# Optimization experiments

Hardware: AMD Instinct MI355X
Metric: run time of the kernel (lower is better)

The kernel has to match this reference:

```python
import jax, jax.numpy as jnp
import numpy as np

DIM = 16      # model width (hardcoded in source)
HEADS = 4
DH = DIM // HEADS  # 4, per-head dim
MLP = 4
L = 4         # encoder layers
OUT = 16      # mlp_head output
EPS = 1e-5


def _ln(x, g, b):
    mu = jnp.mean(x, axis=-1, keepdims=True)
    var = jnp.mean((x - mu) ** 2, axis=-1, keepdims=True)
    return (x - mu) * jax.lax.rsqrt(var + EPS) * g + b


def setup_inputs() -> dict:
    key = jax.random.key(0)
    ks = jax.random.split(key, 16)
    B, S = 256, 512
    s = 0.1
    return {
        "x": jax.random.normal(ks[0], (B, S, DIM), jnp.float32),
        "ln1_g": jnp.ones((L, DIM), jnp.float32),
        "ln1_b": jnp.zeros((L, DIM), jnp.float32),
        "in_w": jax.random.normal(ks[1], (L, 3 * DIM, DIM), jnp.float32) * s,
        "in_b": jax.random.normal(ks[2], (L, 3 * DIM), jnp.float32) * s,
        "out_w": jax.random.normal(ks[3], (L, DIM, DIM), jnp.float32) * s,
        "out_b": jax.random.normal(ks[4], (L, DIM), jnp.float32) * s,
        "ln2_g": jnp.ones((L, DIM), jnp.float32),
        "ln2_b": jnp.zeros((L, DIM), jnp.float32),
        "w1": jax.random.normal(ks[5], (L, MLP, DIM), jnp.float32) * s,
        "b1": jax.random.normal(ks[6], (L, MLP), jnp.float32) * s,
        "w2": jax.random.normal(ks[7], (L, DIM, MLP), jnp.float32) * s,
        "b2": jax.random.normal(ks[8], (L, DIM), jnp.float32) * s,
        "head_g": jnp.ones((DIM,), jnp.float32),
        "head_b": jnp.zeros((DIM,), jnp.float32),
        "head_w": jax.random.normal(ks[9], (OUT, DIM), jnp.float32) * s,
        "head_bias": jax.random.normal(ks[10], (OUT,), jnp.float32) * s,
    }


def reference(x, ln1_g, ln1_b, in_w, in_b, out_w, out_b,
              ln2_g, ln2_b, w1, b1, w2, b2,
              head_g, head_b, head_w, head_bias):
    B, S, _ = x.shape
    scale = 1.0 / np.sqrt(DH)
    for i in range(L):
        # --- pre-LN self-attention + residual (dropout=identity at inference)
        h = _ln(x, ln1_g[i], ln1_b[i])
        qkv = h @ in_w[i].T + in_b[i]                      # [B,S,3*DIM]
        q, k, v = jnp.split(qkv, 3, axis=-1)
        q = q.reshape(B, S, HEADS, DH).transpose(0, 2, 1, 3)  # [B,H,S,Dh]
        k = k.reshape(B, S, HEADS, DH).transpose(0, 2, 1, 3)
        v = v.reshape(B, S, HEADS, DH).transpose(0, 2, 1, 3)
        scores = jnp.einsum('bhsd,bhtd->bhst', q * scale, k)  # [B,H,S,S]
        attn = jax.nn.softmax(scores, axis=-1)
        o = jnp.einsum('bhst,bhtd->bhsd', attn, v)             # [B,H,S,Dh]
        o = o.transpose(0, 2, 1, 3).reshape(B, S, DIM)
        x = x + (o @ out_w[i].T + out_b[i])
        # --- pre-LN MLP + residual (exact GELU, as torch nn.GELU default)
        h = _ln(x, ln2_g[i], ln2_b[i])
        h = jax.nn.gelu(h @ w1[i].T + b1[i], approximate=False)
        x = x + (h @ w2[i].T + b2[i])
    cls = x[:, 0, :]                                          # [B,DIM]
    return _ln(cls, head_g, head_b) @ head_w.T + head_bias    # [B,OUT]
```

## Files before the change

kernel.cpp:

```cpp
#include <hip/hip_runtime.h>
#include <math.h>

#define NDIM 16
#define NMLP 4
#define NL 4
#define NOUT 16
#define NS 512
#define NT 1024
#define LEPS 1e-5f
#define VPAD 516
#define KPAD 28

typedef __fp16 h2 __attribute__((ext_vector_type(2)));
typedef __fp16 h4 __attribute__((ext_vector_type(4)));
typedef __fp16 h8 __attribute__((ext_vector_type(8)));
typedef float f32x4 __attribute__((ext_vector_type(4)));

__device__ __forceinline__ h2 pk2(float x, float y) {
    return __builtin_amdgcn_cvt_pkrtz(x, y);
}

__device__ __forceinline__ float fexp2(float x) {
#if __has_builtin(__builtin_amdgcn_exp2f)
    return __builtin_amdgcn_exp2f(x);
#else
    return exp2f(x);
#endif
}

#define MFMA32(a,b,c) __builtin_amdgcn_mfma_f32_16x16x32_f16((a),(b),(c),0,0,0)

__global__ __launch_bounds__(NT, 4)
void vit_fused(const float* __restrict__ gx,
               const float* __restrict__ g_ln1g, const float* __restrict__ g_ln1b,
               const float* __restrict__ g_inw,  const float* __restrict__ g_inb,
               const float* __restrict__ g_outw, const float* __restrict__ g_outb,
               const float* __restrict__ g_ln2g, const float* __restrict__ g_ln2b,
               const float* __restrict__ g_w1,   const float* __restrict__ g_b1,
               const float* __restrict__ g_w2,   const float* __restrict__ g_b2,
               const float* __restrict__ g_hg,   const float* __restrict__ g_hb,
               const float* __restrict__ g_hw,   const float* __restrict__ g_hbias,
               float* __restrict__ gout)
{
    __shared__ __align__(16) __fp16 sKh[NS][KPAD];
    __shared__ __align__(16) __fp16 sVT[NDIM][VPAD];
    __shared__ __align__(16) __fp16 sQO[NS][NDIM];
    __shared__ __align__(16) float sWiw[NL*48*NDIM];
    __shared__ float sWib[NL*48];
    __shared__ __align__(16) float sWow[NL*NDIM*NDIM];
    __shared__ float sWob[NL*NDIM];
    __shared__ float sLn1g[NL*NDIM], sLn1b[NL*NDIM], sLn2g[NL*NDIM], sLn2b[NL*NDIM];
    __shared__ __align__(16) float sW1[NL*NMLP*NDIM];
    __shared__ float sB1[NL*NMLP];
    __shared__ __align__(16) float sW2[NL*NDIM*NMLP];
    __shared__ float sB2[NL*NDIM];
    __shared__ float sHg[NDIM], sHb[NDIM];
    __shared__ __align__(16) float sHw[NOUT*NDIM];
    __shared__ float sHbias[NOUT];

    const int tid = threadIdx.x;
    const int t   = tid & (NS-1);
    const int hb  = (tid >> 9) << 3;
    const int b   = blockIdx.x;

    const int w  = tid >> 6;
    const int l  = tid & 63;
    const int g  = l >> 4;
    const int ql = l & 15;
    const int r0 = 32*w;

    for (int i = tid; i < NL*48*NDIM; i += NT) sWiw[i] = g_inw[i];
    for (int i = tid; i < NL*48;       i += NT) sWib[i] = g_inb[i];
    for (int i = tid; i < NL*NDIM*NDIM; i += NT) sWow[i] = g_outw[i];
    if (tid < NL*NDIM) {
        sWob[tid]  = g_outb[tid];
        sLn1g[tid] = g_ln1g[tid];  sLn1b[tid] = g_ln1b[tid];
        sLn2g[tid] = g_ln2g[tid];  sLn2b[tid] = g_ln2b[tid];
        sB2[tid]   = g_b2[tid];
    }
    for (int i = tid; i < NL*NMLP*NDIM; i += NT) { sW1[i] = g_w1[i]; sW2[i] = g_w2[i]; }
    if (tid < NL*NMLP) sB1[tid] = g_b1[tid];
    if (tid < NDIM)  { sHg[tid] = g_hg[tid]; sHb[tid] = g_hb[tid]; }
    if (tid < NOUT)    sHbias[tid] = g_hbias[tid];
    for (int i = tid; i < NOUT*NDIM; i += NT) sHw[i] = g_hw[i];

    float xr[NDIM];
    {
        const float4* xg4 = (const float4*)(gx + ((size_t)b*NS + t)*NDIM);
        float4 a = xg4[0], b4 = xg4[1], c4 = xg4[2], d4 = xg4[3];
        xr[0]=a.x;  xr[1]=a.y;  xr[2]=a.z;  xr[3]=a.w;
        xr[4]=b4.x; xr[5]=b4.y; xr[6]=b4.z; xr[7]=b4.w;
        xr[8]=c4.x; xr[9]=c4.y; xr[10]=c4.z; xr[11]=c4.w;
        xr[12]=d4.x; xr[13]=d4.y; xr[14]=d4.z; xr[15]=d4.w;
    }

    __syncthreads();

    for (int li = 0; li < NL; ++li) {
        float mu = 0.f;
        #pragma unroll
        for (int c = 0; c < NDIM; ++c) mu += xr[c];
        mu *= (1.f/NDIM);
        float var = 0.f;
        #pragma unroll
        for (int c = 0; c < NDIM; ++c) { float d = xr[c]-mu; var += d*d; }
        var *= (1.f/NDIM);
        float rs = rsqrtf(var + LEPS);
        float hn[NDIM];
        #pragma unroll
        for (int c = 0; c < NDIM; ++c)
            hn[c] = (xr[c]-mu)*rs*sLn1g[li*NDIM+c] + sLn1b[li*NDIM+c];

        const float* iw = &sWiw[li*48*NDIM];
        const float* ib = &sWib[li*48];

        {
            const float C = 0.72134752044448170368f;
            float qf[8];
            #pragma unroll
            for (int r = 0; r < 8; ++r) {
                const float* wrow = &iw[(hb+r)*NDIM];
                float acc = ib[hb+r];
                #pragma unroll
                for (int c = 0; c < NDIM; ++c) acc += hn[c]*wrow[c];
                qf[r] = acc*C;
            }
            h4 qlo = __builtin_shufflevector(pk2(qf[0],qf[1]), pk2(qf[2],qf[3]), 0,1,2,3);
            h4 qhi = __builtin_shufflevector(pk2(qf[4],qf[5]), pk2(qf[6],qf[7]), 0,1,2,3);
            *(h4*)&sQO[t][hb]   = qlo;
            *(h4*)&sQO[t][hb+4] = qhi;
        }
        {
            float kr[8];
            #pragma unroll
            for (int r = 0; r < 8; ++r) {
                const float* wrow = &iw[(16+hb+r)*NDIM];
                float acc = ib[16+hb+r];
                #pragma unroll
                for (int c = 0; c < NDIM; ++c) acc += hn[c]*wrow[c];
                kr[r] = acc;
            }
            h4 klo = __builtin_shufflevector(pk2(kr[0],kr[1]), pk2(kr[2],kr[3]), 0,1,2,3);
            h4 khi = __builtin_shufflevector(pk2(kr[4],kr[5]), pk2(kr[6],kr[7]), 0,1,2,3);
            *(h4*)&sKh[t][hb]   = klo;
            *(h4*)&sKh[t][hb+4] = khi;
        }
        {
            #pragma unroll
            for (int r = 0; r < 8; ++r) {
                const float* wrow = &iw[(32+hb+r)*NDIM];
                float acc = ib[32+hb+r];
                #pragma unroll
                for (int c = 0; c < NDIM; ++c) acc += hn[c]*wrow[c];
                sVT[hb+r][t] = (__fp16)acc;
            }
        }
        __syncthreads();

        {
            h4 z4 = {};
            h8 z8 = {};
            h8 ones8 = {(__fp16)1.f,(__fp16)1.f,(__fp16)1.f,(__fp16)1.f,
                        (__fp16)1.f,(__fp16)1.f,(__fp16)1.f,(__fp16)1.f};
            h4 q4a = *(const h4*)&sQO[r0 + ql][4*g];
            h4 q4b = *(const h4*)&sQO[r0 + 16 + ql][4*g];
            h8 q8a = __builtin_shufflevector(q4a, z4, 0,1,2,3,4,5,6,7);
            h8 q8b = __builtin_shufflevector(q4b, z4, 0,1,2,3,4,5,6,7);
            h8 bqa[4], bqb[4];
            #pragma unroll
            for (int h = 0; h < 4; ++h) {
                bqa[h] = (g == h) ? q8a : z8;
                bqb[h] = (g == h) ? q8b : z8;
            }
            f32x4 zc = {0.f, 0.f, 0.f, 0.f};
            f32x4 acc[2][4];
            f32x4 sacc[2][4];
            #pragma unroll
            for (int qt = 0; qt < 2; ++qt)
                #pragma unroll
                for (int h = 0; h < 4; ++h) { acc[qt][h] = zc; sacc[qt][h] = zc; }

            for (int jj = 0; jj < NS; jj += 32) {
                h4 ak0 = *(const h4*)&sKh[jj + ql][4*g];
                h4 ak1 = *(const h4*)&sKh[jj + 16 + ql][4*g];
                h8 a0 = __builtin_shufflevector(ak0, z4, 0,1,2,3,4,5,6,7);
                h8 a1 = __builtin_shufflevector(ak1, z4, 0,1,2,3,4,5,6,7);
                h4 av0 = *(const h4*)&sVT[ql][jj + 4*g];
                h4 av1 = *(const h4*)&sVT[ql][jj + 16 + 4*g];
                h8 av  = __builtin_shufflevector(av0, av1, 0,1,2,3,4,5,6,7);

                #pragma unroll
                for (int h = 0; h < 4; ++h) {
                    {
                        f32x4 T0 = MFMA32(a0, bqa[h], zc);
                        f32x4 T1 = MFMA32(a1, bqa[h], zc);
                        h2 r0h = pk2(fexp2(T0[0]), fexp2(T0[1]));
                        h2 r1h = pk2(fexp2(T0[2]), fexp2(T0[3]));
                        h2 r2h = pk2(fexp2(T1[0]), fexp2(T1[1]));
                        h2 r3h = pk2(fexp2(T1[2]), fexp2(T1[3]));
                        h8 pb = __builtin_shufflevector(
                                    __builtin_shufflevector(r0h, r1h, 0,1,2,3),
                                    __builtin_shufflevector(r2h, r3h, 0,1,2,3),
                                    0,1,2,3,4,5,6,7);
                        acc[0][h]  = MFMA32(av, pb, acc[0][h]);
                        sacc[0][h] = MFMA32(ones8, pb, sacc[0][h]);
                    }
                    {
                        f32x4 T0 = MFMA32(a0, bqb[h], zc);
                        f32x4 T1 = MFMA32(a1, bqb[h], zc);
                        h2 r0h = pk2(fexp2(T0[0]), fexp2(T0[1]));
                        h2 r1h = pk2(fexp2(T0[2]), fexp2(T0[3]));
                        h2 r2h = pk2(fexp2(T1[0]), fexp2(T1[1]));
                        h2 r3h = pk2(fexp2(T1[2]), fexp2(T1[3]));
                        h8 pb = __builtin_shufflevector(
                                    __builtin_shufflevector(r0h, r1h, 0,1,2,3),
                                    __builtin_shufflevector(r2h, r3h, 0,1,2,3),
                                    0,1,2,3,4,5,6,7);
                        acc[1][h]  = MFMA32(av, pb, acc[1][h]);
                        sacc[1][h] = MFMA32(ones8, pb, sacc[1][h]);
                    }
                }
            }

            #pragma unroll
            for (int qt = 0; qt < 2; ++qt) {
                float sg = (g < 2) ? ((g == 0) ? sacc[qt][0][0] : sacc[qt][1][0])
                                   : ((g == 2) ? sacc[qt][2][0] : sacc[qt][3][0]);
                f32x4 C = (g < 2) ? ((g == 0) ? acc[qt][0] : acc[qt][1])
                                  : ((g == 2) ? acc[qt][2] : acc[qt][3]);
                float inv = 1.f / sg;
                h4 o4 = __builtin_shufflevector(pk2(C[0]*inv, C[1]*inv),
                                                pk2(C[2]*inv, C[3]*inv), 0,1,2,3);
                *(h4*)&sQO[r0 + 16*qt + ql][4*g] = o4;
            }
        }
        __syncthreads();

        float of[NDIM];
        {
            float4 lo = *(const float4*)&sQO[t][0];
            float4 hi = *(const float4*)&sQO[t][8];
            const h2* l2  = (const h2*)&lo;
            const h2* h2p = (const h2*)&hi;
            #pragma unroll
            for (int i = 0; i < 4; ++i) {
                of[2*i]     = (float)l2[i].x;  of[2*i+1]   = (float)l2[i].y;
                of[8+2*i]   = (float)h2p[i].x; of[8+2*i+1] = (float)h2p[i].y;
            }
        }
        __syncthreads();

        {
            const float* ow = &sWow[li*NDIM*NDIM];
            const float* ob = &sWob[li*NDIM];
            #pragma unroll
            for (int c = 0; c < NDIM; ++c) {
                float acc = ob[c];
                #pragma unroll
                for (int k = 0; k < NDIM; ++k) acc += of[k]*ow[c*NDIM+k];
                xr[c] += acc;
            }
        }
        {
            float mu2 = 0.f;
            #pragma unroll
            for (int c = 0; c < NDIM; ++c) mu2 += xr[c];
            mu2 *= (1.f/NDIM);
            float var2 = 0.f;
            #pragma unroll
            for (int c = 0; c < NDIM; ++c) { float d = xr[c]-mu2; var2 += d*d; }
            var2 *= (1.f/NDIM);
            float rs2 = rsqrtf(var2 + LEPS);
            float hn2[NDIM];
            #pragma unroll
            for (int c = 0; c < NDIM; ++c)
                hn2[c] = (xr[c]-mu2)*rs2*sLn2g[li*NDIM+c] + sLn2b[li*NDIM+c];

            const float* w1p = &sW1[li*NMLP*NDIM];
            float h1[NMLP];
            #pragma unroll
            for (int m = 0; m < NMLP; ++m) {
                float acc = sB1[li*NMLP+m];
                #pragma unroll
                for (int c = 0; c < NDIM; ++c) acc += hn2[c]*w1p[m*NDIM+c];
                h1[m] = 0.5f*acc*(1.f + erff(acc*0.70710678118654752f));
            }
            const float* w2p = &sW2[li*NDIM*NMLP];
            #pragma unroll
            for (int c = 0; c < NDIM; ++c) {
                float acc = sB2[li*NDIM+c];
                #pragma unroll
                for (int m = 0; m < NMLP; ++m) acc += h1[m]*w2p[c*NMLP+m];
                xr[c] += acc;
            }
        }
    }

    if (tid == 0) {
        float mu = 0.f;
        #pragma unroll
        for (int c = 0; c < NDIM; ++c) mu += xr[c];
        mu *= (1.f/NDIM);
        float var = 0.f;
        #pragma unroll
        for (int c = 0; c < NDIM; ++c) { float d = xr[c]-mu; var += d*d; }
        var *= (1.f/NDIM);
        float rs = rsqrtf(var + LEPS);
        float hn[NDIM];
        #pragma unroll
        for (int c = 0; c < NDIM; ++c)
            hn[c] = (xr[c]-mu)*rs*sHg[c] + sHb[c];
        #pragma unroll
        for (int oi = 0; oi < NOUT; ++oi) {
            float acc = sHbias[oi];
            #pragma unroll
            for (int c = 0; c < NDIM; ++c) acc += hn[c]*sHw[oi*NDIM+c];
            gout[b*NOUT + oi] = acc;
        }
    }
}

extern "C" void kernel_launch(void* const* d_in, const int* in_sizes, int n_in,
                              void* d_out, int out_size, void* d_ws, size_t ws_size,
                              hipStream_t stream) {
    const float* x       = (const float*)d_in[0];
    const float* ln1_g   = (const float*)d_in[1];
    const float* ln1_b   = (const float*)d_in[2];
    const float* in_w    = (const float*)d_in[3];
    const float* in_b    = (const float*)d_in[4];
    const float* out_w   = (const float*)d_in[5];
    const float* out_b   = (const float*)d_in[6];
    const float* ln2_g   = (const float*)d_in[7];
    const float* ln2_b   = (const float*)d_in[8];
    const float* w1      = (const float*)d_in[9];
    const float* b1      = (const float*)d_in[10];
    const float* w2      = (const float*)d_in[11];
    const float* b2      = (const float*)d_in[12];
    const float* head_g  = (const float*)d_in[13];
    const float* head_b  = (const float*)d_in[14];
    const float* head_w  = (const float*)d_in[15];
    const float* head_bias = (const float*)d_in[16];
    float* out = (float*)d_out;

    const int B = in_sizes[0] / (NS * NDIM);

    vit_fused<<<B, NT, 0, stream>>>(x, ln1_g, ln1_b, in_w, in_b, out_w, out_b,
                                    ln2_g, ln2_b, w1, b1, w2, b2,
                                    head_g, head_b, head_w, head_bias, out);
}
```

Measured before the change: 177.2 us.

## Process the two query tiles sequentially in attention to cut live registers

The attention block used to handle both 16-row query tiles inside each K/V sweep, keeping two sets of accumulators and Q fragments live. It now loops over the query tiles with unroll 1 and re-reads the K/V fragments from LDS for each tile, which halves the accumulator registers. The aim is lower VGPR pressure and possibly higher occupancy, paid for by loading K and V from shared memory twice and having less independent MFMA work in flight per iteration.

```diff
diff --git a/kernel.cpp b/kernel.cpp
--- a/kernel.cpp
+++ b/kernel.cpp
@@ -157,28 +157,23 @@
         }
         __syncthreads();
 
-        {
+        #pragma unroll 1
+        for (int qt = 0; qt < 2; ++qt) {
             h4 z4 = {};
             h8 z8 = {};
             h8 ones8 = {(__fp16)1.f,(__fp16)1.f,(__fp16)1.f,(__fp16)1.f,
                         (__fp16)1.f,(__fp16)1.f,(__fp16)1.f,(__fp16)1.f};
-            h4 q4a = *(const h4*)&sQO[r0 + ql][4*g];
-            h4 q4b = *(const h4*)&sQO[r0 + 16 + ql][4*g];
-            h8 q8a = __builtin_shufflevector(q4a, z4, 0,1,2,3,4,5,6,7);
-            h8 q8b = __builtin_shufflevector(q4b, z4, 0,1,2,3,4,5,6,7);
-            h8 bqa[4], bqb[4];
-            #pragma unroll
-            for (int h = 0; h < 4; ++h) {
-                bqa[h] = (g == h) ? q8a : z8;
-                bqb[h] = (g == h) ? q8b : z8;
-            }
+            h4 q4 = *(const h4*)&sQO[r0 + 16*qt + ql][4*g];
+            h8 q8 = __builtin_shufflevector(q4, z4, 0,1,2,3,4,5,6,7);
+            h8 bq[4];
+            #pragma unroll
+            for (int h = 0; h < 4; ++h) bq[h] = (g == h) ? q8 : z8;
+
             f32x4 zc = {0.f, 0.f, 0.f, 0.f};
-            f32x4 acc[2][4];
-            f32x4 sacc[2][4];
-            #pragma unroll
-            for (int qt = 0; qt < 2; ++qt)
-                #pragma unroll
-                for (int h = 0; h < 4; ++h) { acc[qt][h] = zc; sacc[qt][h] = zc; }
+            f32x4 acc[4];
+            f32x4 sacc[4];
+            #pragma unroll
+            for (int h = 0; h < 4; ++h) { acc[h] = zc; sacc[h] = zc; }
 
             for (int jj = 0; jj < NS; jj += 32) {
                 h4 ak0 = *(const h4*)&sKh[jj + ql][4*g];
@@ -191,48 +186,29 @@
 
                 #pragma unroll
                 for (int h = 0; h < 4; ++h) {
-                    {
-                        f32x4 T0 = MFMA32(a0, bqa[h], zc);
-                        f32x4 T1 = MFMA32(a1, bqa[h], zc);
-                        h2 r0h = pk2(fexp2(T0[0]), fexp2(T0[1]));
-                        h2 r1h = pk2(fexp2(T0[2]), fexp2(T0[3]));
-                        h2 r2h = pk2(fexp2(T1[0]), fexp2(T1[1]));
-                        h2 r3h = pk2(fexp2(T1[2]), fexp2(T1[3]));
-                        h8 pb = __builtin_shufflevector(
-                                    __builtin_shufflevector(r0h, r1h, 0,1,2,3),
-                                    __builtin_shufflevector(r2h, r3h, 0,1,2,3),
-                                    0,1,2,3,4,5,6,7);
-                        acc[0][h]  = MFMA32(av, pb, acc[0][h]);
-                        sacc[0][h] = MFMA32(ones8, pb, sacc[0][h]);
-                    }
-                    {
-                        f32x4 T0 = MFMA32(a0, bqb[h], zc);
-                        f32x4 T1 = MFMA32(a1, bqb[h], zc);
-                        h2 r0h = pk2(fexp2(T0[0]), fexp2(T0[1]));
-                        h2 r1h = pk2(fexp2(T0[2]), fexp2(T0[3]));
-                        h2 r2h = pk2(fexp2(T1[0]), fexp2(T1[1]));
-                        h2 r3h = pk2(fexp2(T1[2]), fexp2(T1[3]));
-                        h8 pb = __builtin_shufflevector(
-                                    __builtin_shufflevector(r0h, r1h, 0,1,2,3),
-                                    __builtin_shufflevector(r2h, r3h, 0,1,2,3),
-                                    0,1,2,3,4,5,6,7);
-                        acc[1][h]  = MFMA32(av, pb, acc[1][h]);
-                        sacc[1][h] = MFMA32(ones8, pb, sacc[1][h]);
-                    }
+                    f32x4 T0 = MFMA32(a0, bq[h], zc);
+                    f32x4 T1 = MFMA32(a1, bq[h], zc);
+                    h2 r0h = pk2(fexp2(T0[0]), fexp2(T0[1]));
+                    h2 r1h = pk2(fexp2(T0[2]), fexp2(T0[3]));
+                    h2 r2h = pk2(fexp2(T1[0]), fexp2(T1[1]));
+                    h2 r3h = pk2(fexp2(T1[2]), fexp2(T1[3]));
+                    h8 pb = __builtin_shufflevector(
+                                __builtin_shufflevector(r0h, r1h, 0,1,2,3),
+                                __builtin_shufflevector(r2h, r3h, 0,1,2,3),
+                                0,1,2,3,4,5,6,7);
+                    acc[h]  = MFMA32(av, pb, acc[h]);
+                    sacc[h] = MFMA32(ones8, pb, sacc[h]);
                 }
             }
 
-            #pragma unroll
-            for (int qt = 0; qt < 2; ++qt) {
-                float sg = (g < 2) ? ((g == 0) ? sacc[qt][0][0] : sacc[qt][1][0])
-                                   : ((g == 2) ? sacc[qt][2][0] : sacc[qt][3][0]);
-                f32x4 C = (g < 2) ? ((g == 0) ? acc[qt][0] : acc[qt][1])
-                                  : ((g == 2) ? acc[qt][2] : acc[qt][3]);
-                float inv = 1.f / sg;
-                h4 o4 = __builtin_shufflevector(pk2(C[0]*inv, C[1]*inv),
-                                                pk2(C[2]*inv, C[3]*inv), 0,1,2,3);
-                *(h4*)&sQO[r0 + 16*qt + ql][4*g] = o4;
-            }
+            float sg = (g < 2) ? ((g == 0) ? sacc[0][0] : sacc[1][0])
+                               : ((g == 2) ? sacc[2][0] : sacc[3][0]);
+            f32x4 C = (g < 2) ? ((g == 0) ? acc[0] : acc[1])
+                              : ((g == 2) ? acc[2] : acc[3]);
+            float inv = 1.f / sg;
+            h4 o4 = __builtin_shufflevector(pk2(C[0]*inv, C[1]*inv),
+                                            pk2(C[2]*inv, C[3]*inv), 0,1,2,3);
+            *(h4*)&sQO[r0 + 16*qt + ql][4*g] = o4;
         }
         __syncthreads();
 
```

New measurement: 170.1 us (median of 2 runs). -4.0%, faster.
